# Performance work log

Hardware: AMD Instinct MI355X
Metric: run time of the kernel (lower is better)

The kernel has to match this reference:

```python
import jax, jax.numpy as jnp
import numpy as np

B, T, E, H, HD, FF = 2, 2048, 1024, 16, 64, 4096
LN_EPS = 1e-5


def _ln(x, g, b):
    mu = jnp.mean(x, axis=-1, keepdims=True)
    var = jnp.var(x, axis=-1, keepdims=True)
    return (x - mu) * jax.lax.rsqrt(var + LN_EPS) * g + b


def setup_inputs() -> dict:
    key = jax.random.key(0)
    ks = jax.random.split(key, 8)
    s = 0.02
    return {
        "x": jax.random.normal(ks[0], (B, T, E), jnp.float32),
        "Wq": jax.random.normal(ks[1], (H, E, HD), jnp.float32) * s,
        "Wk": jax.random.normal(ks[2], (H, E, HD), jnp.float32) * s,
        "Wv": jax.random.normal(ks[3], (H, E, HD), jnp.float32) * s,
        "Wproj": jax.random.normal(ks[4], (E, E), jnp.float32) * s,
        "bproj": jnp.zeros((E,), jnp.float32),
        "W1": jax.random.normal(ks[5], (E, FF), jnp.float32) * s,
        "b1": jnp.zeros((FF,), jnp.float32),
        "W2": jax.random.normal(ks[6], (FF, E), jnp.float32) * s,
        "b2": jnp.zeros((E,), jnp.float32),
        "g1": jnp.ones((E,), jnp.float32),
        "be1": jnp.zeros((E,), jnp.float32),
        "g2": jnp.ones((E,), jnp.float32),
        "be2": jnp.zeros((E,), jnp.float32),
    }


def reference(x, Wq, Wk, Wv, Wproj, bproj, W1, b1, W2, b2, g1, be1, g2, be2):
    # --- pre-LN multi-head causal self-attention (dropout = eval/identity) ---
    h = _ln(x, g1, be1)  # [B,T,E]
    q = jnp.einsum('btd,hde->bhte', h, Wq)  # [B,H,T,HD]
    k = jnp.einsum('btd,hde->bhte', h, Wk)
    v = jnp.einsum('btd,hde->bhte', h, Wv)
    # NOTE: original code scales by C**-0.5 where C = embedding_dim (not head_size)
    scale = E ** (-0.5)
    wei = jnp.einsum('bhqe,bhke->bhqk', q, k) * scale  # [B,H,T,T]
    causal = jnp.tril(jnp.ones((T, T), dtype=bool))
    wei = jnp.where(causal, wei, -jnp.inf)
    attn = jax.nn.softmax(wei, axis=-1)
    o = jnp.einsum('bhqk,bhke->bhqe', attn, v)  # [B,H,T,HD]
    o = o.transpose(0, 2, 1, 3).reshape(B, T, E)  # concat heads
    o = o @ Wproj + bproj
    x = x + o
    # --- ReLU FFN ---
    h2 = _ln(x, g2, be2)
    f = jax.nn.relu(h2 @ W1 + b1) @ W2 + b2
    return x + f
```

## Files before the change

### kernel.cpp

```cpp
#include <hip/hip_runtime.h>
#include <hip/hip_bf16.h>
#include <stdint.h>

#define T_SEQ 2048
#define E_DIM 1024
#define H_NUM 16
#define HD_DIM 64
#define FF_DIM 4096
#define B_NUM 2
#define N_TOK (B_NUM * T_SEQ)

typedef unsigned short ushort_t;
typedef __bf16 bf16x8 __attribute__((ext_vector_type(8)));
typedef float f32x4 __attribute__((ext_vector_type(4)));

__device__ __forceinline__ float bf2f(ushort_t u) {
    return __uint_as_float(((unsigned)u) << 16);
}
__device__ __forceinline__ ushort_t f2bf(float f) {
    unsigned u = __float_as_uint(f);
    u += 0x7fffu + ((u >> 16) & 1u);
    return (ushort_t)(u >> 16);
}
__device__ __forceinline__ float bflo(unsigned u) { return __uint_as_float(u << 16); }
__device__ __forceinline__ float bfhi(unsigned u) { return __uint_as_float(u & 0xffff0000u); }

__device__ __forceinline__ void async_copy16(const ushort_t* g, ushort_t* l) {
    __builtin_amdgcn_global_load_lds(
        (__attribute__((address_space(1))) uint32_t*)(ushort_t*)g,
        (__attribute__((address_space(3))) uint32_t*)l, 16, 0, 0);
}

__global__ __launch_bounds__(256) void ln_kernel(const float* __restrict__ x,
                                                 const float* __restrict__ g,
                                                 const float* __restrict__ be,
                                                 ushort_t* __restrict__ out) {
    __shared__ float red[8];
    const int row = blockIdx.x, tid = threadIdx.x;
    const float* xr = x + (size_t)row * E_DIM;
    float4 v = ((const float4*)xr)[tid];
    float s = v.x + v.y + v.z + v.w;
    float sq = v.x * v.x + v.y * v.y + v.z * v.z + v.w * v.w;
    for (int off = 32; off; off >>= 1) {
        s += __shfl_xor(s, off);
        sq += __shfl_xor(sq, off);
    }
    const int wid = tid >> 6, lane = tid & 63;
    if (lane == 0) { red[wid] = s; red[4 + wid] = sq; }
    __syncthreads();
    s = red[0] + red[1] + red[2] + red[3];
    sq = red[4] + red[5] + red[6] + red[7];
    const float mean = s * (1.0f / E_DIM);
    const float var = sq * (1.0f / E_DIM) - mean * mean;
    const float rstd = rsqrtf(var + 1e-5f);
    float4 gv = ((const float4*)g)[tid];
    float4 bv = ((const float4*)be)[tid];
    unsigned o0 = f2bf((v.x - mean) * rstd * gv.x + bv.x);
    unsigned o1 = f2bf((v.y - mean) * rstd * gv.y + bv.y);
    unsigned o2 = f2bf((v.z - mean) * rstd * gv.z + bv.z);
    unsigned o3 = f2bf((v.w - mean) * rstd * gv.w + bv.w);
    uint2 w;
    w.x = o0 | (o1 << 16);
    w.y = o2 | (o3 << 16);
    ((uint2*)(out + (size_t)row * E_DIM))[tid] = w;
}

__global__ __launch_bounds__(256) void reduce_ln_kernel(const ushort_t* __restrict__ p0,
                                                        const ushort_t* __restrict__ p1,
                                                        const float* __restrict__ x,
                                                        const float* __restrict__ bias,
                                                        const float* __restrict__ g,
                                                        const float* __restrict__ be,
                                                        float* __restrict__ x1,
                                                        ushort_t* __restrict__ h2) {
    __shared__ float red[8];
    const int row = blockIdx.x, tid = threadIdx.x;
    uint2 u0 = ((const uint2*)(p0 + (size_t)row * E_DIM))[tid];
    uint2 u1 = ((const uint2*)(p1 + (size_t)row * E_DIM))[tid];
    float4 xv = ((const float4*)(x + (size_t)row * E_DIM))[tid];
    float4 bv = ((const float4*)bias)[tid];
    float4 v;
    v.x = xv.x + bv.x + bflo(u0.x) + bflo(u1.x);
    v.y = xv.y + bv.y + bfhi(u0.x) + bfhi(u1.x);
    v.z = xv.z + bv.z + bflo(u0.y) + bflo(u1.y);
    v.w = xv.w + bv.w + bfhi(u0.y) + bfhi(u1.y);
    ((float4*)(x1 + (size_t)row * E_DIM))[tid] = v;
    float s = v.x + v.y + v.z + v.w;
    float sq = v.x * v.x + v.y * v.y + v.z * v.z + v.w * v.w;
    for (int off = 32; off; off >>= 1) {
        s += __shfl_xor(s, off);
        sq += __shfl_xor(sq, off);
    }
    const int wid = tid >> 6, lane = tid & 63;
    if (lane == 0) { red[wid] = s; red[4 + wid] = sq; }
    __syncthreads();
    s = red[0] + red[1] + red[2] + red[3];
    sq = red[4] + red[5] + red[6] + red[7];
    const float mean = s * (1.0f / E_DIM);
    const float var = sq * (1.0f / E_DIM) - mean * mean;
    const float rstd = rsqrtf(var + 1e-5f);
    float4 gv = ((const float4*)g)[tid];
    float4 ev = ((const float4*)be)[tid];
    unsigned o0 = f2bf((v.x - mean) * rstd * gv.x + ev.x);
    unsigned o1 = f2bf((v.y - mean) * rstd * gv.y + ev.y);
    unsigned o2 = f2bf((v.z - mean) * rstd * gv.z + ev.z);
    unsigned o3 = f2bf((v.w - mean) * rstd * gv.w + ev.w);
    uint2 w;
    w.x = o0 | (o1 << 16);
    w.y = o2 | (o3 << 16);
    ((uint2*)(h2 + (size_t)row * E_DIM))[tid] = w;
}

__global__ __launch_bounds__(256) void reduce_out_kernel(const ushort_t* __restrict__ p0,
                                                         const ushort_t* __restrict__ p1,
                                                         const float* __restrict__ x1,
                                                         const float* __restrict__ bias,
                                                         float* __restrict__ out) {
    const int row = blockIdx.x, tid = threadIdx.x;
    uint2 u0 = ((const uint2*)(p0 + (size_t)row * E_DIM))[tid];
    uint2 u1 = ((const uint2*)(p1 + (size_t)row * E_DIM))[tid];
    float4 xv = ((const float4*)(x1 + (size_t)row * E_DIM))[tid];
    float4 bv = ((const float4*)bias)[tid];
    float4 v;
    v.x = xv.x + bv.x + bflo(u0.x) + bflo(u1.x);
    v.y = xv.y + bv.y + bfhi(u0.x) + bfhi(u1.x);
    v.z = xv.z + bv.z + bflo(u0.y) + bflo(u1.y);
    v.w = xv.w + bv.w + bfhi(u0.y) + bfhi(u1.y);
    ((float4*)(out + (size_t)row * E_DIM))[tid] = v;
}

__global__ __launch_bounds__(256) void transpose_kernel(const float* __restrict__ in,
                                                        ushort_t* __restrict__ out,
                                                        int R, int C) {
    __shared__ ushort_t tile[32][33];
    const int c0 = blockIdx.x * 32, r0 = blockIdx.y * 32;
    const int tx = threadIdx.x, ty = threadIdx.y;
#pragma unroll
    for (int i = 0; i < 32; i += 8) tile[ty + i][tx] = f2bf(in[(size_t)(r0 + ty + i) * C + (c0 + tx)]);
    __syncthreads();
#pragma unroll
    for (int i = 0; i < 32; i += 8) out[(size_t)(c0 + ty + i) * R + (r0 + tx)] = tile[tx][ty + i];
}

__global__ __launch_bounds__(256) void transpose_qkv_kernel(const float* __restrict__ Wq,
                                                            const float* __restrict__ Wk,
                                                            const float* __restrict__ Wv,
                                                            ushort_t* __restrict__ outT) {
    __shared__ ushort_t tile[32][33];
    const int z = blockIdx.z, m = z >> 4, hh = z & 15;
    const float* in = ((m == 0) ? Wq : ((m == 1) ? Wk : Wv)) + (size_t)hh * E_DIM * HD_DIM;
    ushort_t* out = outT + (size_t)(m * E_DIM + hh * HD_DIM) * E_DIM;
    const int c0 = blockIdx.x * 32, r0 = blockIdx.y * 32;
    const int tx = threadIdx.x, ty = threadIdx.y;
#pragma unroll
    for (int i = 0; i < 32; i += 8) tile[ty + i][tx] = f2bf(in[(size_t)(r0 + ty + i) * HD_DIM + (c0 + tx)]);
    __syncthreads();
#pragma unroll
    for (int i = 0; i < 32; i += 8) out[(size_t)(c0 + ty + i) * E_DIM + (r0 + tx)] = tile[tx][ty + i];
}

template <int MODE, int BK>
__global__ __launch_bounds__(256) void gemm_bt(const ushort_t* __restrict__ A,
                                               const ushort_t* __restrict__ BT,
                                               const float* __restrict__ bias,
                                               const float* __restrict__ resid,
                                               void* __restrict__ C0,
                                               ushort_t* __restrict__ C1,
                                               ushort_t* __restrict__ C2,
                                               int M, int N, int K, int lda) {
    __shared__ __align__(16) ushort_t lds_a[2][128 * BK];
    __shared__ __align__(16) ushort_t lds_b[2][128 * BK];
    const int tid = threadIdx.x;
    const int id = blockIdx.y * gridDim.x + blockIdx.x;
    const int band = id & 7, within = id >> 3;
    const int rpb = gridDim.y >> 3;
    const int by = band * rpb + (within % rpb);
    const int bx = within / rpb;
    const int m0 = by * 128, n0 = bx * 128;
    const int koff = blockIdx.z * K;
    const int wave = tid >> 6, lane = tid & 63;
    const int wm = (wave >> 1) * 64, wn = (wave & 1) * 64;
    const int quad = lane >> 4, l16 = lane & 15;
    f32x4 acc[4][4] = {};

    const int nk = K / BK;
    auto stage = [&](int kt, int buf) {
        const int k0 = koff + kt * BK;
#pragma unroll
        for (int it = 0; it < BK / 16; ++it) {
            const int ci = it * 256 + tid;
            const int kk = ci >> 9;
            const int rem = ci & 511;
            const int r = rem >> 2, kc = rem & 3;
            const int gk = k0 + kk * 32 + kc * 8;
            async_copy16(A + (size_t)(m0 + r) * lda + gk, &lds_a[buf][ci * 8]);
            async_copy16(BT + (size_t)(n0 + r) * lda + gk, &lds_b[buf][ci * 8]);
        }
    };
    stage(0, 0);

#pragma unroll 1
    for (int kt = 0; kt < nk; ++kt) {
        __syncthreads();
        if (kt + 1 < nk) stage(kt + 1, (kt + 1) & 1);
        const ushort_t* la = lds_a[kt & 1];
        const ushort_t* lb = lds_b[kt & 1];
#pragma unroll
        for (int kk = 0; kk < BK / 32; ++kk) {
            const ushort_t* lak = la + kk * 4096;
            const ushort_t* lbk = lb + kk * 4096;
            bf16x8 af[4], bfr[4];
#pragma unroll
            for (int i = 0; i < 4; i++) af[i] = *(const bf16x8*)&lak[(wm + i * 16 + l16) * 32 + quad * 8];
#pragma unroll
            for (int i = 0; i < 4; i++) bfr[i] = *(const bf16x8*)&lbk[(wn + i * 16 + l16) * 32 + quad * 8];
#pragma unroll
            for (int im = 0; im < 4; im++)
#pragma unroll
                for (int in = 0; in < 4; in++)
                    acc[im][in] = __builtin_amdgcn_mfma_f32_16x16x32_bf16(af[im], bfr[in], acc[im][in], 0, 0, 0);
        }
    }

    ushort_t* pc = nullptr;
    if (MODE == 3) pc = (blockIdx.z == 0) ? (ushort_t*)C0 : C1;
#pragma unroll
    for (int im = 0; im < 4; im++) {
#pragma unroll
        for (int in = 0; in < 4; in++) {
            const int col = n0 + wn + in * 16 + l16;
            float bv = (MODE == 1) ? bias[col] : 0.0f;
#pragma unroll
            for (int r = 0; r < 4; r++) {
                const int row = m0 + wm + im * 16 + quad * 4 + r;
                float v = acc[im][in][r] + bv;
                if (MODE == 1) {
                    v += resid[(size_t)row * N + col];
                    ((float*)C0)[(size_t)row * N + col] = v;
                } else {
                    pc[(size_t)row * N + col] = f2bf(v);
                }
            }
        }
    }
    (void)M; (void)C2;
}

template <int MODE>
__global__ __launch_bounds__(512, 2) void gemm256(const ushort_t* __restrict__ A,
                                                  const ushort_t* __restrict__ BT,
                                                  const float* __restrict__ bias,
                                                  void* __restrict__ C0,
                                                  ushort_t* __restrict__ C1,
                                                  ushort_t* __restrict__ C2,
                                                  int N, int K, int lda) {
    __shared__ __align__(16) ushort_t lds_a[2][16384];
    __shared__ __align__(16) ushort_t lds_b[2][16384];
    const int tid = threadIdx.x;
    const int id = blockIdx.y * gridDim.x + blockIdx.x;
    const int band = id & 7, within = id >> 3;
    const int rpb = gridDim.y >> 3;
    const int by = band * rpb + (within % rpb);
    const int bx = within / rpb;
    const int m0 = by * 256, n0 = bx * 256;
    const int wave = tid >> 6, lane = tid & 63;
    const int wr = wave >> 2, wc = wave & 3;
    const int quad = lane >> 4, l16 = lane & 15;
    const int nkt = K >> 6;

    f32x4 acc[8][4] = {};

    auto stageA = [&](int kt, int half) {
        ushort_t* dst = &lds_a[kt & 1][half * 8192];
        const ushort_t* src = A + (size_t)(m0 + half * 128) * lda + kt * 64;
#pragma unroll
        for (int it = 0; it < 2; ++it) {
            const int ci = it * 512 + tid;
            const int r = ci >> 3, c = ci & 7;
            async_copy16(src + (size_t)r * lda + ((c ^ (r & 7)) << 3), dst + ci * 8);
        }
    };
    auto stageB = [&](int kt, int half) {
        ushort_t* dst = &lds_b[kt & 1][half * 8192];
        const ushort_t* src = BT + (size_t)(n0 + half * 128) * lda + kt * 64;
#pragma unroll
        for (int it = 0; it < 2; ++it) {
            const int ci = it * 512 + tid;
            const int r = ci >> 3, c = ci & 7;
            async_copy16(src + (size_t)r * lda + ((c ^ (r & 7)) << 3), dst + ci * 8);
        }
    };

    stageA(0, 0); stageA(0, 1);
    stageB(0, 0); stageB(0, 1);
    stageB(1, 0); stageB(1, 1);
    asm volatile("s_waitcnt vmcnt(4)" ::: "memory");
    __builtin_amdgcn_s_barrier();

    const int swz = l16 & 7;

#pragma unroll 1
    for (int kt = 0; kt < nkt; ++kt) {
        const int buf = kt & 1;
        const ushort_t* la = &lds_a[buf][wr * 8192];
        const ushort_t* lb = &lds_b[buf][(wc >> 1) * 8192];
        const int brow = (wc & 1) * 64;
        bf16x8 bfrag[2][4];
#pragma unroll
        for (int p = 0; p < 4; ++p) {
            bf16x8 af[2][2];
#pragma unroll
            for (int s = 0; s < 2; ++s) {
                const int r = (p * 2 + s) * 16 + l16;
#pragma unroll
                for (int kk = 0; kk < 2; ++kk)
                    af[s][kk] = *(const bf16x8*)&la[r * 64 + (((kk << 2) + quad) ^ swz) * 8];
            }
            if (p == 0) {
#pragma unroll
                for (int kk = 0; kk < 2; ++kk)
#pragma unroll
                    for (int fn = 0; fn < 4; ++fn) {
                        const int r = brow + fn * 16 + l16;
                        bfrag[kk][fn] = *(const bf16x8*)&lb[r * 64 + (((kk << 2) + quad) ^ swz) * 8];
                    }
            }
            if (p == 0) { if (kt + 1 < nkt) stageA(kt + 1, 0); }
            else if (p == 1) { if (kt + 1 < nkt) stageA(kt + 1, 1); }
            else if (p == 2) { if (kt + 2 < nkt) stageB(kt + 2, 0); }
            else { if (kt + 2 < nkt) stageB(kt + 2, 1); }

            __builtin_amdgcn_s_barrier();
            asm volatile("s_waitcnt lgkmcnt(0)" ::: "memory");
            __builtin_amdgcn_sched_barrier(0);
            __builtin_amdgcn_s_setprio(1);
#pragma unroll
            for (int s = 0; s < 2; ++s)
#pragma unroll
                for (int kk = 0; kk < 2; ++kk)
#pragma unroll
                    for (int fn = 0; fn < 4; ++fn)
                        acc[p * 2 + s][fn] = __builtin_amdgcn_mfma_f32_16x16x32_bf16(
                            af[s][kk], bfrag[kk][fn], acc[p * 2 + s][fn], 0, 0, 0);
            __builtin_amdgcn_s_setprio(0);
            if (p == 3) {
                if (kt + 2 < nkt) asm volatile("s_waitcnt vmcnt(4)" ::: "memory");
                else              asm volatile("s_waitcnt vmcnt(0)" ::: "memory");
            }
            __builtin_amdgcn_s_barrier();
        }
    }

#pragma unroll
    for (int fm = 0; fm < 8; ++fm) {
        const int row_base = m0 + wr * 128 + fm * 16 + quad * 4;
#pragma unroll
        for (int fn = 0; fn < 4; ++fn) {
            const int col = n0 + wc * 64 + fn * 16 + l16;
            if (MODE == 2) {
                const float bv = bias[col];
#pragma unroll
                for (int r = 0; r < 4; ++r)
                    ((ushort_t*)C0)[(size_t)(row_base + r) * N + col] =
                        f2bf(fmaxf(acc[fm][fn][r] + bv, 0.0f));
            } else {
                const int mat = col >> 10, c = col & 1023, hh = c >> 6, d = c & 63;
#pragma unroll
                for (int r = 0; r < 4; ++r) {
                    const int row = row_base + r;
                    const int bb = row >> 11, tt = row & 2047;
                    const int bh = bb * H_NUM + hh;
                    float v = acc[fm][fn][r];
                    size_t idx;
                    ushort_t* dst;
                    if (mat == 0) {
                        idx = ((((size_t)bh * 32 + (tt >> 6)) * 8 + (d >> 3)) * 64 + (tt & 63)) * 8 + (d & 7);
                        dst = (ushort_t*)C0;
                        v *= 0.0450842048f;
                    } else if (mat == 1) {
                        idx = ((((size_t)bh * 32 + (tt >> 6)) * 8 + (d >> 3)) * 64 + (tt & 63)) * 8 + (d & 7);
                        dst = C1;
                    } else {
                        idx = ((((size_t)bh * 32 + (tt >> 6)) * 8 + ((tt & 63) >> 3)) * 64 + d) * 8 + (tt & 7);
                        dst = C2;
                    }
                    dst[idx] = f2bf(v);
                }
            }
        }
    }
}

__global__ __launch_bounds__(256, 2) void attn_flash(const ushort_t* __restrict__ qP,
                                                     const ushort_t* __restrict__ kP,
                                                     const ushort_t* __restrict__ vP,
                                                     ushort_t* __restrict__ o) {
    __shared__ __align__(16) ushort_t P_lds[4][32 * 72];
    __shared__ __align__(16) float Ored[2][32][68];
    __shared__ float Lred[2][32];
    const int h = blockIdx.x, p = blockIdx.y, b = blockIdx.z;
    const int bh = b * H_NUM + h;
    const int tid = threadIdx.x;
    const int wave = tid >> 6, lane = tid & 63;
    const int wr = wave >> 1, ws = wave & 1;
    const int quad = lane >> 4, l16 = lane & 15;
    ushort_t* Pw = P_lds[wave];
    const ushort_t* kbase = kP + (size_t)bh * 32 * 4096;
    const ushort_t* vbase = vP + (size_t)bh * 32 * 4096;
    bf16x8 onesf;
#pragma unroll
    for (int j = 0; j < 8; ++j) onesf[j] = (__bf16)1.0f;

#pragma unroll 1
    for (int phase = 0; phase < 2; ++phase) {
        const int qt = (phase == 0) ? (31 - p) : p;
        const int nkt = qt + 1;
        const ushort_t* qbase = qP + ((size_t)bh * 32 + qt) * 4096;
        bf16x8 qf[2][2];
#pragma unroll
        for (int rg = 0; rg < 2; ++rg)
#pragma unroll
            for (int kk = 0; kk < 2; ++kk)
                qf[rg][kk] = *(const bf16x8*)&qbase[((kk * 4 + quad) * 64 + wr * 32 + rg * 16 + l16) * 8];
        f32x4 oacc[2][4] = {};
        f32x4 lacc[2] = {};
        __syncthreads();
        bf16x8 kf[8], vf[8];
        {
            const ushort_t* kb = kbase + (size_t)ws * 4096;
#pragma unroll
            for (int i = 0; i < 8; ++i)
                kf[i] = *(const bf16x8*)&kb[(((i >> 2) * 4 + quad) * 64 + (i & 3) * 16 + l16) * 8];
        }
#pragma unroll 1
        for (int kt = ws; kt < nkt; kt += 2) {
            f32x4 sacc[2][4] = {};
            __builtin_amdgcn_s_setprio(1);
#pragma unroll
            for (int kk = 0; kk < 2; ++kk)
#pragma unroll
                for (int kg = 0; kg < 4; ++kg)
#pragma unroll
                    for (int rg = 0; rg < 2; ++rg)
                        sacc[rg][kg] = __builtin_amdgcn_mfma_f32_16x16x32_bf16(
                            qf[rg][kk], kf[kk * 4 + kg], sacc[rg][kg], 0, 0, 0);
            __builtin_amdgcn_s_setprio(0);
            {
                const ushort_t* vb = vbase + (size_t)kt * 4096;
#pragma unroll
                for (int i = 0; i < 8; ++i)
                    vf[i] = *(const bf16x8*)&vb[(((i >> 2) * 4 + quad) * 64 + (i & 3) * 16 + l16) * 8];
            }
            if (kt + 2 < nkt) {
                const ushort_t* kb = kbase + (size_t)(kt + 2) * 4096;
#pragma unroll
                for (int i = 0; i < 8; ++i)
                    kf[i] = *(const bf16x8*)&kb[(((i >> 2) * 4 + quad) * 64 + (i & 3) * 16 + l16) * 8];
            }
#pragma unroll
            for (int rg = 0; rg < 2; ++rg)
#pragma unroll
                for (int kg = 0; kg < 4; ++kg) {
                    f32x4 sv = sacc[rg][kg];
                    if (kt == qt) {
                        const int jc = kg * 16 + l16;
#pragma unroll
                        for (int r = 0; r < 4; ++r)
                            if (jc > wr * 32 + rg * 16 + quad * 4 + r) sv[r] = -3.0e38f;
                    }
#pragma unroll
                    for (int r = 0; r < 4; ++r) {
                        const float e = exp2f(sv[r]);
                        Pw[(rg * 16 + quad * 4 + r) * 72 + kg * 16 + l16] =
                            (ushort_t)(__float_as_uint(e) >> 16);
                    }
                }
            __builtin_amdgcn_s_setprio(1);
#pragma unroll
            for (int kk = 0; kk < 2; ++kk)
#pragma unroll
                for (int rg = 0; rg < 2; ++rg) {
                    bf16x8 pf = *(const bf16x8*)&Pw[(rg * 16 + l16) * 72 + kk * 32 + quad * 8];
                    lacc[rg] = __builtin_amdgcn_mfma_f32_16x16x32_bf16(pf, onesf, lacc[rg], 0, 0, 0);
#pragma unroll
                    for (int dg = 0; dg < 4; ++dg)
                        oacc[rg][dg] = __builtin_amdgcn_mfma_f32_16x16x32_bf16(
                            pf, vf[kk * 4 + dg], oacc[rg][dg], 0, 0, 0);
                }
            __builtin_amdgcn_s_setprio(0);
        }
        if (ws == 1) {
#pragma unroll
            for (int rg = 0; rg < 2; ++rg) {
#pragma unroll
                for (int dg = 0; dg < 4; ++dg)
#pragma unroll
                    for (int r = 0; r < 4; ++r)
                        Ored[wr][rg * 16 + quad * 4 + r][dg * 16 + l16] = oacc[rg][dg][r];
                if (l16 == 0) {
#pragma unroll
                    for (int r = 0; r < 4; ++r)
                        Lred[wr][rg * 16 + quad * 4 + r] = lacc[rg][r];
                }
            }
        }
        __syncthreads();
        if (ws == 0) {
#pragma unroll
            for (int rg = 0; rg < 2; ++rg)
#pragma unroll
                for (int r = 0; r < 4; ++r) {
                    const int rr = rg * 16 + quad * 4 + r;
                    const float inv = 1.0f / (lacc[rg][r] + Lred[wr][rr]);
                    const int trow = qt * 64 + wr * 32 + rr;
#pragma unroll
                    for (int dg = 0; dg < 4; ++dg) {
                        const float v = oacc[rg][dg][r] + Ored[wr][rr][dg * 16 + l16];
                        o[(size_t)(b * T_SEQ + trow) * E_DIM + h * HD_DIM + dg * 16 + l16] =
                            f2bf(v * inv);
                    }
                }
        }
    }
}

extern "C" void kernel_launch(void* const* d_in, const int* in_sizes, int n_in,
                              void* d_out, int out_size, void* d_ws, size_t ws_size,
                              hipStream_t stream) {
    const float* x = (const float*)d_in[0];
    const float* Wq = (const float*)d_in[1];
    const float* Wk = (const float*)d_in[2];
    const float* Wv = (const float*)d_in[3];
    const float* Wproj = (const float*)d_in[4];
    const float* bproj = (const float*)d_in[5];
    const float* W1 = (const float*)d_in[6];
    const float* b1 = (const float*)d_in[7];
    const float* W2 = (const float*)d_in[8];
    const float* b2 = (const float*)d_in[9];
    const float* g1 = (const float*)d_in[10];
    const float* be1 = (const float*)d_in[11];
    const float* g2 = (const float*)d_in[12];
    const float* be2 = (const float*)d_in[13];

    char* ws = (char*)d_ws;
    const size_t MB = 1024 * 1024;
    ushort_t* W2T    = (ushort_t*)(ws + 0 * MB);
    float*    x1     = (float*)   (ws + 8 * MB);
    ushort_t* W1T    = (ushort_t*)(ws + 24 * MB);
    ushort_t* WprojT = (ushort_t*)(ws + 32 * MB);
    ushort_t* hln    = (ushort_t*)(ws + 34 * MB);
    ushort_t* ocat   = hln;
    ushort_t* WqkvT  = (ushort_t*)(ws + 42 * MB);
    ushort_t* qP     = (ushort_t*)(ws + 48 * MB);
    ushort_t* kP     = (ushort_t*)(ws + 56 * MB);
    ushort_t* vP     = (ushort_t*)(ws + 64 * MB);
    ushort_t* h2     = (ushort_t*)(ws + 72 * MB);
    ushort_t* f1     = (ushort_t*)(ws + 34 * MB);
    ushort_t* pp0    = (ushort_t*)(ws + 48 * MB);
    ushort_t* pp1    = (ushort_t*)(ws + 56 * MB);
    ushort_t* fp0    = (ushort_t*)(ws + 66 * MB);
    ushort_t* fp1    = (ushort_t*)(ws + 24 * MB);
    (void)ws_size; (void)in_sizes; (void)n_in; (void)out_size;

    const dim3 tb(32, 8, 1);
    transpose_qkv_kernel<<<dim3(2, 32, 48), tb, 0, stream>>>(Wq, Wk, Wv, WqkvT);
    transpose_kernel<<<dim3(32, 32, 1), tb, 0, stream>>>(Wproj, WprojT, E_DIM, E_DIM);
    transpose_kernel<<<dim3(128, 32, 1), tb, 0, stream>>>(W1, W1T, E_DIM, FF_DIM);
    transpose_kernel<<<dim3(32, 128, 1), tb, 0, stream>>>(W2, W2T, FF_DIM, E_DIM);

    ln_kernel<<<N_TOK, 256, 0, stream>>>(x, g1, be1, hln);
    gemm256<0><<<dim3(12, 16), 512, 0, stream>>>(hln, WqkvT, nullptr,
                                                 qP, kP, vP, 3 * E_DIM, E_DIM, E_DIM);
    attn_flash<<<dim3(16, 16, 2), 256, 0, stream>>>(qP, kP, vP, ocat);
    gemm_bt<3, 64><<<dim3(8, 32, 2), 256, 0, stream>>>(ocat, WprojT, nullptr, nullptr,
                                                       pp0, pp1, nullptr, N_TOK, E_DIM, 512, E_DIM);
    reduce_ln_kernel<<<N_TOK, 256, 0, stream>>>(pp0, pp1, x, bproj, g2, be2, x1, h2);
    gemm256<2><<<dim3(16, 16), 512, 0, stream>>>(h2, W1T, b1, f1, nullptr, nullptr,
                                                 FF_DIM, E_DIM, E_DIM);
    gemm_bt<3, 64><<<dim3(8, 32, 2), 256, 0, stream>>>(f1, W2T, nullptr, nullptr,
                                                       fp0, fp1, nullptr, N_TOK, E_DIM, 2048, FF_DIM);
    reduce_out_kernel<<<N_TOK, 256, 0, stream>>>(fp0, fp1, x1, b2, (float*)d_out);
}
```

Baseline: 323.3 us.

## Merge weight transposes into one launch and retile QKV GEMM to 256x192

Replaces the four weight-transpose launches with a single kernel that picks its source matrix and tile from a flat block id, removing per-launch overhead. Adds a dedicated QKV GEMM with 256x192 tiles, so the grid grows from 12x16=192 blocks to 16x16=256, filling more compute units on the device. The new GEMM has its own staging schedule (three B chunks per k-step) and writes the packed Q/K/V layouts in its epilogue. The general GEMM epilogue is reduced to the bias+ReLU path. Smaller tiles mean less data reuse per block and different wait counts, which could offset the occupancy gain.

Result: faster. 316.7 us (-2.0%).

```diff
diff --git a/kernel.cpp b/kernel.cpp
--- a/kernel.cpp
+++ b/kernel.cpp
@@ -129,34 +129,47 @@
     ((float4*)(out + (size_t)row * E_DIM))[tid] = v;
 }
 
-__global__ __launch_bounds__(256) void transpose_kernel(const float* __restrict__ in,
-                                                        ushort_t* __restrict__ out,
-                                                        int R, int C) {
+__global__ __launch_bounds__(256) void transpose_all_kernel(const float* __restrict__ Wq,
+                                                            const float* __restrict__ Wk,
+                                                            const float* __restrict__ Wv,
+                                                            const float* __restrict__ Wproj,
+                                                            const float* __restrict__ W1,
+                                                            const float* __restrict__ W2,
+                                                            ushort_t* __restrict__ WqkvT,
+                                                            ushort_t* __restrict__ WprojT,
+                                                            ushort_t* __restrict__ W1T,
+                                                            ushort_t* __restrict__ W2T) {
     __shared__ ushort_t tile[32][33];
-    const int c0 = blockIdx.x * 32, r0 = blockIdx.y * 32;
+    const int id = blockIdx.x;
+    const float* in;
+    ushort_t* out;
+    int R, C, r0, c0;
+    if (id < 3072) {
+        const int z = id >> 6, rem = id & 63;
+        const int m = z >> 4, hh = z & 15;
+        in = ((m == 0) ? Wq : ((m == 1) ? Wk : Wv)) + (size_t)hh * E_DIM * HD_DIM;
+        out = WqkvT + (size_t)(m * E_DIM + hh * HD_DIM) * E_DIM;
+        R = E_DIM; C = HD_DIM;
+        c0 = (rem & 1) * 32; r0 = (rem >> 1) * 32;
+    } else if (id < 4096) {
+        const int i = id - 3072;
+        in = Wproj; out = WprojT; R = E_DIM; C = E_DIM;
+        c0 = (i & 31) * 32; r0 = (i >> 5) * 32;
+    } else if (id < 8192) {
+        const int i = id - 4096;
+        in = W1; out = W1T; R = E_DIM; C = FF_DIM;
+        c0 = (i & 127) * 32; r0 = (i >> 7) * 32;
+    } else {
+        const int i = id - 8192;
+        in = W2; out = W2T; R = FF_DIM; C = E_DIM;
+        c0 = (i & 31) * 32; r0 = (i >> 5) * 32;
+    }
     const int tx = threadIdx.x, ty = threadIdx.y;
 #pragma unroll
     for (int i = 0; i < 32; i += 8) tile[ty + i][tx] = f2bf(in[(size_t)(r0 + ty + i) * C + (c0 + tx)]);
     __syncthreads();
 #pragma unroll
     for (int i = 0; i < 32; i += 8) out[(size_t)(c0 + ty + i) * R + (r0 + tx)] = tile[tx][ty + i];
-}
-
-__global__ __launch_bounds__(256) void transpose_qkv_kernel(const float* __restrict__ Wq,
-                                                            const float* __restrict__ Wk,
-                                                            const float* __restrict__ Wv,
-                                                            ushort_t* __restrict__ outT) {
-    __shared__ ushort_t tile[32][33];
-    const int z = blockIdx.z, m = z >> 4, hh = z & 15;
-    const float* in = ((m == 0) ? Wq : ((m == 1) ? Wk : Wv)) + (size_t)hh * E_DIM * HD_DIM;
-    ushort_t* out = outT + (size_t)(m * E_DIM + hh * HD_DIM) * E_DIM;
-    const int c0 = blockIdx.x * 32, r0 = blockIdx.y * 32;
-    const int tx = threadIdx.x, ty = threadIdx.y;
-#pragma unroll
-    for (int i = 0; i < 32; i += 8) tile[ty + i][tx] = f2bf(in[(size_t)(r0 + ty + i) * HD_DIM + (c0 + tx)]);
-    __syncthreads();
-#pragma unroll
-    for (int i = 0; i < 32; i += 8) out[(size_t)(c0 + ty + i) * E_DIM + (r0 + tx)] = tile[tx][ty + i];
 }
 
 template <int MODE, int BK>
@@ -357,35 +370,145 @@
 #pragma unroll
         for (int fn = 0; fn < 4; ++fn) {
             const int col = n0 + wc * 64 + fn * 16 + l16;
-            if (MODE == 2) {
-                const float bv = bias[col];
-#pragma unroll
-                for (int r = 0; r < 4; ++r)
-                    ((ushort_t*)C0)[(size_t)(row_base + r) * N + col] =
-                        f2bf(fmaxf(acc[fm][fn][r] + bv, 0.0f));
-            } else {
-                const int mat = col >> 10, c = col & 1023, hh = c >> 6, d = c & 63;
-#pragma unroll
-                for (int r = 0; r < 4; ++r) {
-                    const int row = row_base + r;
-                    const int bb = row >> 11, tt = row & 2047;
-                    const int bh = bb * H_NUM + hh;
-                    float v = acc[fm][fn][r];
-                    size_t idx;
-                    ushort_t* dst;
-                    if (mat == 0) {
-                        idx = ((((size_t)bh * 32 + (tt >> 6)) * 8 + (d >> 3)) * 64 + (tt & 63)) * 8 + (d & 7);
-                        dst = (ushort_t*)C0;
-                        v *= 0.0450842048f;
-                    } else if (mat == 1) {
-                        idx = ((((size_t)bh * 32 + (tt >> 6)) * 8 + (d >> 3)) * 64 + (tt & 63)) * 8 + (d & 7);
-                        dst = C1;
-                    } else {
-                        idx = ((((size_t)bh * 32 + (tt >> 6)) * 8 + ((tt & 63) >> 3)) * 64 + d) * 8 + (tt & 7);
-                        dst = C2;
+            const float bv = bias[col];
+#pragma unroll
+            for (int r = 0; r < 4; ++r)
+                ((ushort_t*)C0)[(size_t)(row_base + r) * N + col] =
+                    f2bf(fmaxf(acc[fm][fn][r] + bv, 0.0f));
+        }
+    }
+    (void)C1; (void)C2;
+}
+
+__global__ __launch_bounds__(512, 2) void gemm192_qkv(const ushort_t* __restrict__ A,
+                                                      const ushort_t* __restrict__ BT,
+                                                      ushort_t* __restrict__ qP,
+                                                      ushort_t* __restrict__ kP,
+                                                      ushort_t* __restrict__ vP,
+                                                      int K, int lda) {
+    __shared__ __align__(16) ushort_t lds_a[2][16384];
+    __shared__ __align__(16) ushort_t lds_b[2][12288];
+    const int tid = threadIdx.x;
+    const int id = blockIdx.y * gridDim.x + blockIdx.x;
+    const int band = id & 7, within = id >> 3;
+    const int rpb = gridDim.y >> 3;
+    const int by = band * rpb + (within % rpb);
+    const int bx = within / rpb;
+    const int m0 = by * 256, n0 = bx * 192;
+    const int wave = tid >> 6, lane = tid & 63;
+    const int wr = wave >> 2, wc = wave & 3;
+    const int quad = lane >> 4, l16 = lane & 15;
+    const int nkt = K >> 6;
+
+    f32x4 acc[8][3] = {};
+
+    auto stageA = [&](int kt, int half) {
+        ushort_t* dst = &lds_a[kt & 1][half * 8192];
+        const ushort_t* src = A + (size_t)(m0 + half * 128) * lda + kt * 64;
+#pragma unroll
+        for (int it = 0; it < 2; ++it) {
+            const int ci = it * 512 + tid;
+            const int r = ci >> 3, c = ci & 7;
+            async_copy16(src + (size_t)r * lda + ((c ^ (r & 7)) << 3), dst + ci * 8);
+        }
+    };
+    auto stageB = [&](int kt) {
+        ushort_t* dst = lds_b[kt & 1];
+        const ushort_t* src = BT + (size_t)n0 * lda + kt * 64;
+#pragma unroll
+        for (int it = 0; it < 3; ++it) {
+            const int ci = it * 512 + tid;
+            const int r = ci >> 3, c = ci & 7;
+            async_copy16(src + (size_t)r * lda + ((c ^ (r & 7)) << 3), dst + ci * 8);
+        }
+    };
+
+    stageA(0, 0); stageA(0, 1);
+    stageB(0);
+    stageB(1);
+    asm volatile("s_waitcnt vmcnt(3)" ::: "memory");
+    __builtin_amdgcn_s_barrier();
+
+    const int swz = l16 & 7;
+
+#pragma unroll 1
+    for (int kt = 0; kt < nkt; ++kt) {
+        const int buf = kt & 1;
+        const ushort_t* la = &lds_a[buf][wr * 8192];
+        const ushort_t* lb = lds_b[buf];
+        const int brow = wc * 48;
+        bf16x8 bfrag[2][3];
+#pragma unroll
+        for (int p = 0; p < 4; ++p) {
+            bf16x8 af[2][2];
+#pragma unroll
+            for (int s = 0; s < 2; ++s) {
+                const int r = (p * 2 + s) * 16 + l16;
+#pragma unroll
+                for (int kk = 0; kk < 2; ++kk)
+                    af[s][kk] = *(const bf16x8*)&la[r * 64 + (((kk << 2) + quad) ^ swz) * 8];
+            }
+            if (p == 0) {
+#pragma unroll
+                for (int kk = 0; kk < 2; ++kk)
+#pragma unroll
+                    for (int fn = 0; fn < 3; ++fn) {
+                        const int r = brow + fn * 16 + l16;
+                        bfrag[kk][fn] = *(const bf16x8*)&lb[r * 64 + (((kk << 2) + quad) ^ swz) * 8];
                     }
-                    dst[idx] = f2bf(v);
+            }
+            if (p == 0) { if (kt + 1 < nkt) stageA(kt + 1, 0); }
+            else if (p == 1) { if (kt + 1 < nkt) stageA(kt + 1, 1); }
+            else if (p == 2) { if (kt + 2 < nkt) stageB(kt + 2); }
+
+            __builtin_amdgcn_s_barrier();
+            asm volatile("s_waitcnt lgkmcnt(0)" ::: "memory");
+            __builtin_amdgcn_sched_barrier(0);
+            __builtin_amdgcn_s_setprio(1);
+#pragma unroll
+            for (int s = 0; s < 2; ++s)
+#pragma unroll
+                for (int kk = 0; kk < 2; ++kk)
+#pragma unroll
+                    for (int fn = 0; fn < 3; ++fn)
+                        acc[p * 2 + s][fn] = __builtin_amdgcn_mfma_f32_16x16x32_bf16(
+                            af[s][kk], bfrag[kk][fn], acc[p * 2 + s][fn], 0, 0, 0);
+            __builtin_amdgcn_s_setprio(0);
+            if (p == 3) {
+                if (kt + 2 < nkt) asm volatile("s_waitcnt vmcnt(3)" ::: "memory");
+                else              asm volatile("s_waitcnt vmcnt(0)" ::: "memory");
+            }
+            __builtin_amdgcn_s_barrier();
+        }
+    }
+
+#pragma unroll
+    for (int fm = 0; fm < 8; ++fm) {
+        const int row_base = m0 + wr * 128 + fm * 16 + quad * 4;
+#pragma unroll
+        for (int fn = 0; fn < 3; ++fn) {
+            const int col = n0 + wc * 48 + fn * 16 + l16;
+            const int mat = col >> 10, c = col & 1023, hh = c >> 6, d = c & 63;
+#pragma unroll
+            for (int r = 0; r < 4; ++r) {
+                const int row = row_base + r;
+                const int bb = row >> 11, tt = row & 2047;
+                const int bh = bb * H_NUM + hh;
+                float v = acc[fm][fn][r];
+                size_t idx;
+                ushort_t* dst;
+                if (mat == 0) {
+                    idx = ((((size_t)bh * 32 + (tt >> 6)) * 8 + (d >> 3)) * 64 + (tt & 63)) * 8 + (d & 7);
+                    dst = qP;
+                    v *= 0.0450842048f;
+                } else if (mat == 1) {
+                    idx = ((((size_t)bh * 32 + (tt >> 6)) * 8 + (d >> 3)) * 64 + (tt & 63)) * 8 + (d & 7);
+                    dst = kP;
+                } else {
+                    idx = ((((size_t)bh * 32 + (tt >> 6)) * 8 + ((tt & 63) >> 3)) * 64 + d) * 8 + (tt & 7);
+                    dst = vP;
                 }
+                dst[idx] = f2bf(v);
             }
         }
     }
@@ -562,15 +685,11 @@
     ushort_t* fp1    = (ushort_t*)(ws + 24 * MB);
     (void)ws_size; (void)in_sizes; (void)n_in; (void)out_size;
 
-    const dim3 tb(32, 8, 1);
-    transpose_qkv_kernel<<<dim3(2, 32, 48), tb, 0, stream>>>(Wq, Wk, Wv, WqkvT);
-    transpose_kernel<<<dim3(32, 32, 1), tb, 0, stream>>>(Wproj, WprojT, E_DIM, E_DIM);
-    transpose_kernel<<<dim3(128, 32, 1), tb, 0, stream>>>(W1, W1T, E_DIM, FF_DIM);
-    transpose_kernel<<<dim3(32, 128, 1), tb, 0, stream>>>(W2, W2T, FF_DIM, E_DIM);
+    transpose_all_kernel<<<12288, dim3(32, 8, 1), 0, stream>>>(
+        Wq, Wk, Wv, Wproj, W1, W2, WqkvT, WprojT, W1T, W2T);
 
     ln_kernel<<<N_TOK, 256, 0, stream>>>(x, g1, be1, hln);
-    gemm256<0><<<dim3(12, 16), 512, 0, stream>>>(hln, WqkvT, nullptr,
-                                                 qP, kP, vP, 3 * E_DIM, E_DIM, E_DIM);
+    gemm192_qkv<<<dim3(16, 16), 512, 0, stream>>>(hln, WqkvT, qP, kP, vP, E_DIM, E_DIM);
     attn_flash<<<dim3(16, 16, 2), 256, 0, stream>>>(qP, kP, vP, ocat);
     gemm_bt<3, 64><<<dim3(8, 32, 2), 256, 0, stream>>>(ocat, WprojT, nullptr, nullptr,
                                                        pp0, pp1, nullptr, N_TOK, E_DIM, 512, E_DIM);
```
